# Optimization experiments

Measured on AMD Instinct MI355X. Metric: run time of the kernel, lower is better.

Reference implementation:

```python
import jax, jax.numpy as jnp
import numpy as np

D_MODEL = 1024
NHEAD = 16
HEAD_DIM = D_MODEL // NHEAD
WINDOW = 64


def setup_inputs() -> dict:
    key = jax.random.key(0)
    ks = jax.random.split(key, 5)
    B, S = 1, 4096
    x = jax.random.normal(ks[0], (B, S, D_MODEL), dtype=jnp.float32)
    scale = 0.02
    Wq = jax.random.normal(ks[1], (D_MODEL, D_MODEL), dtype=jnp.float32) * scale
    Wk = jax.random.normal(ks[2], (D_MODEL, D_MODEL), dtype=jnp.float32) * scale
    Wv = jax.random.normal(ks[3], (D_MODEL, D_MODEL), dtype=jnp.float32) * scale
    Wo = jax.random.normal(ks[4], (D_MODEL, D_MODEL), dtype=jnp.float32) * scale
    return {"x": x, "Wq": Wq, "Wk": Wk, "Wv": Wv, "Wo": Wo}


def reference(x, Wq, Wk, Wv, Wo):
    B, S, D = x.shape
    H, hd, W = NHEAD, HEAD_DIM, WINDOW
    # projections (torch Linear: y = x @ W.T)
    q = (x @ Wq.T).reshape(B, S, H, hd).transpose(0, 2, 1, 3)  # [B,H,S,hd]
    k = (x @ Wk.T).reshape(B, S, H, hd).transpose(0, 2, 1, 3)
    v = (x @ Wv.T).reshape(B, S, H, hd).transpose(0, 2, 1, 3)
    # sliding window indices: each query attends to [i-W+1, i]
    qpos = jnp.arange(S)
    offsets = jnp.arange(-W + 1, 1)
    key_idx = qpos[:, None] + offsets[None, :]          # [S,W]
    valid = (key_idx >= 0) & (key_idx < S)
    key_idx = jnp.clip(key_idx, 0, S - 1)
    # gather windows: [B,H,S,W,hd]
    kw = jnp.take(k, key_idx, axis=2)
    vw = jnp.take(v, key_idx, axis=2)
    scores = jnp.einsum('bhsd,bhswd->bhsw', q, kw) / (hd ** 0.5)
    scores = jnp.where(valid[None, None, :, :], scores, -jnp.inf)
    attn = jax.nn.softmax(scores, axis=-1)
    out = jnp.einsum('bhsw,bhswd->bhsd', attn, vw)      # [B,H,S,hd]
    out = out.transpose(0, 2, 1, 3).reshape(B, S, D)
    return out @ Wo.T
```

## Files before the change

kernel.cpp:

```cpp
#include <hip/hip_runtime.h>
#include <cstdint>

typedef unsigned short u16;
using bf16x8 = __attribute__((ext_vector_type(8))) short;
using u16x8  = __attribute__((ext_vector_type(8))) unsigned short;
using f32x4  = __attribute__((ext_vector_type(4))) float;

#define DM 1024

__device__ __forceinline__ u16 f2b(float f) {
    union { float f; unsigned u; } v; v.f = f;
    unsigned r = v.u + 0x7FFFu + ((v.u >> 16) & 1u);
    return (u16)(r >> 16);
}
__device__ __forceinline__ float b2f(u16 b) {
    union { unsigned u; float f; } v; v.u = ((unsigned)b) << 16;
    return v.f;
}

#define GLL(gp, lp) __builtin_amdgcn_global_load_lds( \
    (const __attribute__((address_space(1))) void*)(uintptr_t)(gp), \
    (__attribute__((address_space(3))) void*)(unsigned)(uintptr_t)(lp), 16, 0, 0)

#define BAR()    __builtin_amdgcn_s_barrier()
#define WAITV3() asm volatile("s_waitcnt vmcnt(3)" ::: "memory")
#define WAITV0() asm volatile("s_waitcnt vmcnt(0)" ::: "memory")

__global__ __launch_bounds__(256) void cvt_all(const float* __restrict__ x,
                                               const float* __restrict__ Wq,
                                               const float* __restrict__ Wk,
                                               const float* __restrict__ Wv,
                                               const float* __restrict__ Wo,
                                               u16* __restrict__ xb,
                                               u16* __restrict__ wqkv,
                                               u16* __restrict__ wob) {
    size_t v = ((size_t)blockIdx.x * 256 + threadIdx.x) << 3;
    const float* src; u16* dst; size_t off;
    if (v < (size_t)4194304) { src = x; dst = xb; off = v; }
    else {
        size_t w = v - 4194304; int s = (int)(w >> 20); off = w & 1048575;
        src = (s == 0) ? Wq : (s == 1) ? Wk : (s == 2) ? Wv : Wo;
        dst = (s < 3) ? (wqkv + ((size_t)s << 20)) : wob;
    }
    const f32x4* p = (const f32x4*)(src + off);
    f32x4 a = p[0], b = p[1];
    u16x8 o;
    o[0] = f2b(a[0]); o[1] = f2b(a[1]); o[2] = f2b(a[2]); o[3] = f2b(a[3]);
    o[4] = f2b(b[0]); o[5] = f2b(b[1]); o[6] = f2b(b[2]); o[7] = f2b(b[3]);
    *(u16x8*)(dst + off) = o;
}

#define MROW3(af_, bf_, d) \
    acc[d][0] = __builtin_amdgcn_mfma_f32_16x16x32_bf16(af_, bf_[0], acc[d][0], 0, 0, 0); \
    acc[d][1] = __builtin_amdgcn_mfma_f32_16x16x32_bf16(af_, bf_[1], acc[d][1], 0, 0, 0); \
    acc[d][2] = __builtin_amdgcn_mfma_f32_16x16x32_bf16(af_, bf_[2], acc[d][2], 0, 0, 0);

#define MFMA12(af_, bf_, ib) do { \
    __builtin_amdgcn_s_setprio(1); \
    MROW3(af_[0], bf_, (ib) + 0) \
    MROW3(af_[1], bf_, (ib) + 1) \
    MROW3(af_[2], bf_, (ib) + 2) \
    MROW3(af_[3], bf_, (ib) + 3) \
    __builtin_amdgcn_s_setprio(0); } while (0)

__global__ __launch_bounds__(512, 2) void gemm_qkv8(const u16* __restrict__ A,
                                                    const u16* __restrict__ B,
                                                    u16* __restrict__ QKV) {
    __shared__ __align__(16) u16 As[2 * 16384];
    __shared__ __align__(16) u16 Bs[2 * 12288];
    const int tid  = threadIdx.x;
    const int lane = tid & 63;
    const int wid  = tid >> 6;
    const int wr   = wid >> 2;
    const int wc   = wid & 3;
    const int fr   = lane & 15;
    const int fg   = lane >> 4;

    const int hw   = blockIdx.y * 16 + blockIdx.x;
    const int lg   = (hw & 7) * 32 + (hw >> 3);
    const int brow = (lg >> 4) << 8;
    const int bcol = (lg & 15) * 192;

    const int srow = tid >> 3;
    const int scol = ((tid & 7) ^ (srow & 7)) << 3;
    const u16* Ag = A + (size_t)(brow + srow) * 1024 + scol;
    const u16* Bg = B + (size_t)(bcol + srow) * 1024 + scol;

#define STG_A(buf, kt, c) GLL(Ag + (size_t)(c) * 65536 + (kt) * 64, \
                              (char*)As + (buf) * 32768 + (c) * 8192 + (wid << 10))
#define STG_B(buf, kt, c) GLL(Bg + (size_t)(c) * 65536 + (kt) * 64, \
                              (char*)Bs + (buf) * 24576 + (c) * 8192 + (wid << 10))

    const int swz  = (fr & 7) << 3;
    const int col0 = (fg << 3) ^ swz;
    const int col1 = (32 + (fg << 3)) ^ swz;
    const int aro  = ((wr << 7) + fr) << 6;
    const int bro  = ((wc * 48) + fr) << 6;

#define LDA4(dst, bufo, ih, cl) do { \
    const u16* p_ = As + (bufo) + aro + ((ih) << 12) + (cl); \
    dst[0] = *(const bf16x8*)(p_); \
    dst[1] = *(const bf16x8*)(p_ + 1024); \
    dst[2] = *(const bf16x8*)(p_ + 2048); \
    dst[3] = *(const bf16x8*)(p_ + 3072); } while (0)

#define LDB3(dst, bufo, cl) do { \
    const u16* p_ = Bs + (bufo) + bro + (cl); \
    dst[0] = *(const bf16x8*)(p_); \
    dst[1] = *(const bf16x8*)(p_ + 1024); \
    dst[2] = *(const bf16x8*)(p_ + 2048); } while (0)

    f32x4 acc[8][3];
    const f32x4 z = {0.f, 0.f, 0.f, 0.f};
    #pragma unroll
    for (int i = 0; i < 8; ++i)
        #pragma unroll
        for (int j = 0; j < 3; ++j) acc[i][j] = z;

    bf16x8 af0[4], af1[4], bf0[3], bf1[3];

    STG_B(0, 0, 0); STG_B(0, 0, 1); STG_B(0, 0, 2);
    STG_A(0, 0, 0); STG_A(0, 0, 1); STG_A(0, 0, 2); STG_A(0, 0, 3);
    STG_B(1, 1, 0); STG_B(1, 1, 1); STG_B(1, 1, 2);
    WAITV3();
    BAR();

    #pragma unroll 1
    for (int t = 0; t < 7; ++t) {
        const int k1 = 2 * t + 1, k2 = 2 * t + 2, k3 = 2 * t + 3;
        LDA4(af0, 0, 0, col0); LDB3(bf0, 0, col0);
        STG_A(1, k1, 0); STG_A(1, k1, 1);
        BAR(); MFMA12(af0, bf0, 0); BAR();
        LDA4(af1, 0, 0, col1); LDB3(bf1, 0, col1);
        STG_A(1, k1, 2); STG_A(1, k1, 3);
        BAR(); MFMA12(af1, bf1, 0); BAR();
        LDA4(af0, 0, 1, col0);
        STG_B(0, k2, 0); STG_B(0, k2, 1);
        BAR(); MFMA12(af0, bf0, 4); BAR();
        LDA4(af1, 0, 1, col1);
        STG_B(0, k2, 2);
        BAR(); MFMA12(af1, bf1, 4); WAITV3(); BAR();
        LDA4(af0, 16384, 0, col0); LDB3(bf0, 12288, col0);
        STG_A(0, k2, 0); STG_A(0, k2, 1);
        BAR(); MFMA12(af0, bf0, 0); BAR();
        LDA4(af1, 16384, 0, col1); LDB3(bf1, 12288, col1);
        STG_A(0, k2, 2); STG_A(0, k2, 3);
        BAR(); MFMA12(af1, bf1, 0); BAR();
        LDA4(af0, 16384, 1, col0);
        STG_B(1, k3, 0); STG_B(1, k3, 1);
        BAR(); MFMA12(af0, bf0, 4); BAR();
        LDA4(af1, 16384, 1, col1);
        STG_B(1, k3, 2);
        BAR(); MFMA12(af1, bf1, 4); WAITV3(); BAR();
    }
    LDA4(af0, 0, 0, col0); LDB3(bf0, 0, col0);
    STG_A(1, 15, 0); STG_A(1, 15, 1);
    BAR(); MFMA12(af0, bf0, 0); BAR();
    LDA4(af1, 0, 0, col1); LDB3(bf1, 0, col1);
    STG_A(1, 15, 2); STG_A(1, 15, 3);
    BAR(); MFMA12(af1, bf1, 0); BAR();
    LDA4(af0, 0, 1, col0);
    BAR(); MFMA12(af0, bf0, 4); BAR();
    LDA4(af1, 0, 1, col1);
    BAR(); MFMA12(af1, bf1, 4); WAITV0(); BAR();
    LDA4(af0, 16384, 0, col0); LDB3(bf0, 12288, col0);
    BAR(); MFMA12(af0, bf0, 0); BAR();
    LDA4(af1, 16384, 0, col1); LDB3(bf1, 12288, col1);
    BAR(); MFMA12(af1, bf1, 0); BAR();
    LDA4(af0, 16384, 1, col0);
    BAR(); MFMA12(af0, bf0, 4); BAR();
    LDA4(af1, 16384, 1, col1);
    BAR(); MFMA12(af1, bf1, 4);

    const int ocol0 = bcol + wc * 48;
    const int orow0 = brow + (wr << 7);
    #pragma unroll
    for (int i = 0; i < 8; ++i)
        #pragma unroll
        for (int j = 0; j < 3; ++j)
            #pragma unroll
            for (int r = 0; r < 4; ++r) {
                const int row = orow0 + i * 16 + fg * 4 + r;
                const int col = ocol0 + j * 16 + fr;
                QKV[(size_t)row * 3072 + col] = f2b(acc[i][j][r]);
            }
#undef STG_A
#undef STG_B
#undef LDA4
#undef LDB3
}

__global__ __launch_bounds__(256) void gemm_out(const u16* __restrict__ A,
                                                const u16* __restrict__ B,
                                                float* __restrict__ C) {
    __shared__ __align__(16) u16 As[2 * 8192];
    __shared__ __align__(16) u16 Bs[2 * 4096];
    const int tid  = threadIdx.x;
    const int lane = tid & 63;
    const int wid  = tid >> 6;
    const int wr   = wid >> 1;
    const int wc   = wid & 1;
    const int fr   = lane & 15;
    const int fg   = lane >> 4;

    const int hw   = blockIdx.y * 16 + blockIdx.x;
    const int lg   = (hw & 7) * 64 + (hw >> 3);
    const int brow = (lg >> 4) << 7;
    const int bcol = (lg & 15) << 6;

    const int srow = tid >> 3;
    const int scol = ((tid & 7) ^ (srow & 7)) << 3;
    const u16* Ag = A + (size_t)(brow + srow) * 1024 + scol;
    const u16* Bg = B + (size_t)(bcol + srow) * 1024 + scol;

#define OSTG_A(buf, kt, c) GLL(Ag + (size_t)(c) * 32768 + (kt) * 64, \
                               (char*)As + (buf) * 16384 + (c) * 4096 + (tid << 4))
#define OSTG_B(buf, kt, c) GLL(Bg + (size_t)(c) * 32768 + (kt) * 64, \
                               (char*)Bs + (buf) * 8192 + (c) * 4096 + (tid << 4))
#define OSTG(buf, kt) do { \
        OSTG_A(buf, kt, 0); OSTG_A(buf, kt, 1); OSTG_A(buf, kt, 2); OSTG_A(buf, kt, 3); \
        OSTG_B(buf, kt, 0); OSTG_B(buf, kt, 1); } while (0)

    const int swz  = (fr & 7) << 3;
    const int col0 = (fg << 3) ^ swz;
    const int col1 = (32 + (fg << 3)) ^ swz;
    const int aro  = ((wr << 6) + fr) << 6;
    const int bro  = ((wc << 5) + fr) << 6;

    f32x4 acc[4][2];
    const f32x4 z = {0.f, 0.f, 0.f, 0.f};
    #pragma unroll
    for (int i = 0; i < 4; ++i) { acc[i][0] = z; acc[i][1] = z; }

    OSTG(0, 0);
    #pragma unroll 2
    for (int kt = 0; kt < 16; ++kt) {
        const int buf = kt & 1;
        __syncthreads();
        if (kt + 1 < 16) OSTG(buf ^ 1, kt + 1);
        const u16* Ab = As + (buf << 13);
        const u16* Bb = Bs + (buf << 12);
        bf16x8 a0[4], a1[4], b0[2], b1[2];
        #pragma unroll
        for (int i = 0; i < 4; ++i) {
            a0[i] = *(const bf16x8*)(Ab + aro + (i << 10) + col0);
            a1[i] = *(const bf16x8*)(Ab + aro + (i << 10) + col1);
        }
        #pragma unroll
        for (int j = 0; j < 2; ++j) {
            b0[j] = *(const bf16x8*)(Bb + bro + (j << 10) + col0);
            b1[j] = *(const bf16x8*)(Bb + bro + (j << 10) + col1);
        }
        #pragma unroll
        for (int i = 0; i < 4; ++i)
            #pragma unroll
            for (int j = 0; j < 2; ++j) {
                acc[i][j] = __builtin_amdgcn_mfma_f32_16x16x32_bf16(a0[i], b0[j], acc[i][j], 0, 0, 0);
                acc[i][j] = __builtin_amdgcn_mfma_f32_16x16x32_bf16(a1[i], b1[j], acc[i][j], 0, 0, 0);
            }
    }
#undef OSTG_A
#undef OSTG_B
#undef OSTG

    #pragma unroll
    for (int i = 0; i < 4; ++i)
        #pragma unroll
        for (int j = 0; j < 2; ++j)
            #pragma unroll
            for (int r = 0; r < 4; ++r) {
                const int row = brow + wr * 64 + i * 16 + fg * 4 + r;
                const int col = bcol + wc * 32 + j * 16 + fr;
                C[(size_t)row * 1024 + col] = acc[i][j][r];
            }
}

__global__ __launch_bounds__(256) void attn_kernel(const u16* __restrict__ QKV,
                                                   u16* __restrict__ Og) {
    const int qb  = blockIdx.x;
    const int h   = blockIdx.y;
    const int tid = threadIdx.x;
    const int lane = tid & 63;
    const int w  = tid >> 6;
    const int fr = lane & 15;
    const int fg = lane >> 4;

    __shared__ __align__(16) u16 QK[64 * 72 + 128 * 72];
    __shared__ __align__(16) u16 Vt[64 * 138];
    __shared__ float Mrow[64][4];
    __shared__ float Lrow[64][4];

    u16* Qs = QK;
    u16* Ks = QK + 64 * 72;
    u16* Ps = QK;

    const u16* Qg = QKV;
    const u16* Kg = QKV + 1024;
    const u16* Vg = QKV + 2048;

    const int hoff  = h * 64;
    const int qrow0 = qb * 64;
    const int krow0 = qrow0 - 64;

    {
        const int r  = tid >> 3;
        const int c0 = (tid & 7) * 8;
        #pragma unroll
        for (int it = 0; it < 2; ++it) {
            const int row = r + it * 32;
            u16x8 val = *(const u16x8*)(Qg + (size_t)(qrow0 + row) * 3072 + hoff + c0);
            u16x8 o;
            #pragma unroll
            for (int e = 0; e < 8; ++e) o[e] = f2b(b2f(val[e]) * 0.125f);
            *(u16x8*)(Qs + row * 72 + c0) = o;
        }
        #pragma unroll
        for (int it = 0; it < 4; ++it) {
            const int row  = r + it * 32;
            const int grow = krow0 + row;
            u16x8 val = {0, 0, 0, 0, 0, 0, 0, 0};
            if (grow >= 0) val = *(const u16x8*)(Kg + (size_t)grow * 3072 + hoff + c0);
            *(u16x8*)(Ks + row * 72 + c0) = val;
        }
        #pragma unroll
        for (int it = 0; it < 4; ++it) {
            const int j    = r + it * 32;
            const int grow = krow0 + j;
            u16x8 val = {0, 0, 0, 0, 0, 0, 0, 0};
            if (grow >= 0) val = *(const u16x8*)(Vg + (size_t)grow * 3072 + hoff + c0);
            #pragma unroll
            for (int e = 0; e < 8; ++e) Vt[(c0 + e) * 138 + j] = val[e];
        }
    }
    __syncthreads();

    const f32x4 z = {0.f, 0.f, 0.f, 0.f};
    f32x4 s[4][2];
    #pragma unroll
    for (int i = 0; i < 4; ++i) { s[i][0] = z; s[i][1] = z; }
    #pragma unroll
    for (int kk = 0; kk < 2; ++kk) {
        const int k0 = kk * 32 + fg * 8;
        bf16x8 aq[4];
        #pragma unroll
        for (int i = 0; i < 4; ++i)
            aq[i] = *(const bf16x8*)(Qs + (i * 16 + fr) * 72 + k0);
        #pragma unroll
        for (int n = 0; n < 2; ++n) {
            const bf16x8 bk = *(const bf16x8*)(Ks + (w * 32 + n * 16 + fr) * 72 + k0);
            #pragma unroll
            for (int i = 0; i < 4; ++i)
                s[i][n] = __builtin_amdgcn_mfma_f32_16x16x32_bf16(aq[i], bk, s[i][n], 0, 0, 0);
        }
    }

    #pragma unroll
    for (int i = 0; i < 4; ++i) {
        #pragma unroll
        for (int r = 0; r < 4; ++r) {
            const int irow = i * 16 + fg * 4 + r;
            float mx = -3.0e38f;
            #pragma unroll
            for (int n = 0; n < 2; ++n) {
                const int jcol = w * 32 + n * 16 + fr;
                const bool valid = (jcol >= irow + 1) && (jcol <= irow + 64) && (krow0 + jcol >= 0);
                const float v = valid ? s[i][n][r] : -3.0e38f;
                s[i][n][r] = v;
                mx = fmaxf(mx, v);
            }
            #pragma unroll
            for (int d = 1; d < 16; d <<= 1) mx = fmaxf(mx, __shfl_xor(mx, d));
            if (fr == 0) Mrow[irow][w] = mx;
        }
    }
    __syncthreads();

    #pragma unroll
    for (int i = 0; i < 4; ++i) {
        #pragma unroll
        for (int r = 0; r < 4; ++r) {
            const int irow = i * 16 + fg * 4 + r;
            const float M = fmaxf(fmaxf(Mrow[irow][0], Mrow[irow][1]),
                                  fmaxf(Mrow[irow][2], Mrow[irow][3]));
            float sum = 0.f;
            #pragma unroll
            for (int n = 0; n < 2; ++n) {
                const float v = s[i][n][r];
                const float p = (v > -1.0e38f) ? __expf(v - M) : 0.f;
                sum += p;
                Ps[irow * 136 + (w * 32 + n * 16 + fr)] = f2b(p);
            }
            #pragma unroll
            for (int d = 1; d < 16; d <<= 1) sum += __shfl_xor(sum, d);
            if (fr == 0) Lrow[irow][w] = sum;
        }
    }
    __syncthreads();

    f32x4 o[4] = {z, z, z, z};
    #pragma unroll
    for (int ks = 0; ks < 4; ++ks) {
        const int k0 = ks * 32 + fg * 8;
        const bf16x8 ap = *(const bf16x8*)(Ps + (w * 16 + fr) * 136 + k0);
        #pragma unroll
        for (int n = 0; n < 4; ++n) {
            const bf16x8 bv = *(const bf16x8*)(Vt + (n * 16 + fr) * 138 + k0);
            o[n] = __builtin_amdgcn_mfma_f32_16x16x32_bf16(ap, bv, o[n], 0, 0, 0);
        }
    }

    #pragma unroll
    for (int r = 0; r < 4; ++r) {
        const int irow = w * 16 + fg * 4 + r;
        const float L = Lrow[irow][0] + Lrow[irow][1] + Lrow[irow][2] + Lrow[irow][3];
        const float rl = 1.0f / L;
        #pragma unroll
        for (int n = 0; n < 4; ++n)
            Og[(size_t)(qrow0 + irow) * DM + hoff + n * 16 + fr] = f2b(o[n][r] * rl);
    }
}

extern "C" void kernel_launch(void* const* d_in, const int* in_sizes, int n_in,
                              void* d_out, int out_size, void* d_ws, size_t ws_size,
                              hipStream_t stream) {
    (void)in_sizes; (void)n_in; (void)out_size; (void)ws_size;
    const float* x  = (const float*)d_in[0];
    const float* Wq = (const float*)d_in[1];
    const float* Wk = (const float*)d_in[2];
    const float* Wv = (const float*)d_in[3];
    const float* Wo = (const float*)d_in[4];
    float* out = (float*)d_out;

    char* ws = (char*)d_ws;
    u16* xb   = (u16*)(ws);
    u16* Wqkv = (u16*)(ws + ((size_t)8  << 20));
    u16* Wob  = (u16*)(ws + ((size_t)14 << 20));
    u16* qkvb = (u16*)(ws + ((size_t)16 << 20));
    u16* ab   = (u16*)(ws + ((size_t)40 << 20));

    cvt_all<<<4096, 256, 0, stream>>>(x, Wq, Wk, Wv, Wo, xb, Wqkv, Wob);
    gemm_qkv8<<<dim3(16, 16), 512, 0, stream>>>(xb, Wqkv, qkvb);
    attn_kernel<<<dim3(64, 16), 256, 0, stream>>>(qkvb, ab);
    gemm_out<<<dim3(16, 32), 256, 0, stream>>>(ab, Wob, out);
}
```

Baseline: 80.79 us.

## Restructure QKV GEMM main loop into simpler double-buffered pipeline, fold Q scale into Wq

```diff
diff --git a/kernel.cpp b/kernel.cpp
--- a/kernel.cpp
+++ b/kernel.cpp
@@ -23,7 +23,7 @@
     (__attribute__((address_space(3))) void*)(unsigned)(uintptr_t)(lp), 16, 0, 0)
 
 #define BAR()    __builtin_amdgcn_s_barrier()
-#define WAITV3() asm volatile("s_waitcnt vmcnt(3)" ::: "memory")
+#define WAITV7() asm volatile("s_waitcnt vmcnt(7)" ::: "memory")
 #define WAITV0() asm volatile("s_waitcnt vmcnt(0)" ::: "memory")
 
 __global__ __launch_bounds__(256) void cvt_all(const float* __restrict__ x,
@@ -35,18 +35,19 @@
                                                u16* __restrict__ wqkv,
                                                u16* __restrict__ wob) {
     size_t v = ((size_t)blockIdx.x * 256 + threadIdx.x) << 3;
-    const float* src; u16* dst; size_t off;
+    const float* src; u16* dst; size_t off; float sc = 1.0f;
     if (v < (size_t)4194304) { src = x; dst = xb; off = v; }
     else {
         size_t w = v - 4194304; int s = (int)(w >> 20); off = w & 1048575;
         src = (s == 0) ? Wq : (s == 1) ? Wk : (s == 2) ? Wv : Wo;
         dst = (s < 3) ? (wqkv + ((size_t)s << 20)) : wob;
+        if (s == 0) sc = 0.125f;
     }
     const f32x4* p = (const f32x4*)(src + off);
     f32x4 a = p[0], b = p[1];
     u16x8 o;
-    o[0] = f2b(a[0]); o[1] = f2b(a[1]); o[2] = f2b(a[2]); o[3] = f2b(a[3]);
-    o[4] = f2b(b[0]); o[5] = f2b(b[1]); o[6] = f2b(b[2]); o[7] = f2b(b[3]);
+    o[0] = f2b(a[0] * sc); o[1] = f2b(a[1] * sc); o[2] = f2b(a[2] * sc); o[3] = f2b(a[3] * sc);
+    o[4] = f2b(b[0] * sc); o[5] = f2b(b[1] * sc); o[6] = f2b(b[2] * sc); o[7] = f2b(b[3] * sc);
     *(u16x8*)(dst + off) = o;
 }
 
@@ -55,12 +56,16 @@
     acc[d][1] = __builtin_amdgcn_mfma_f32_16x16x32_bf16(af_, bf_[1], acc[d][1], 0, 0, 0); \
     acc[d][2] = __builtin_amdgcn_mfma_f32_16x16x32_bf16(af_, bf_[2], acc[d][2], 0, 0, 0);
 
-#define MFMA12(af_, bf_, ib) do { \
+#define MFMA24(ib) do { \
     __builtin_amdgcn_s_setprio(1); \
-    MROW3(af_[0], bf_, (ib) + 0) \
-    MROW3(af_[1], bf_, (ib) + 1) \
-    MROW3(af_[2], bf_, (ib) + 2) \
-    MROW3(af_[3], bf_, (ib) + 3) \
+    MROW3(af0[0], bf0, (ib) + 0) \
+    MROW3(af0[1], bf0, (ib) + 1) \
+    MROW3(af0[2], bf0, (ib) + 2) \
+    MROW3(af0[3], bf0, (ib) + 3) \
+    MROW3(af1[0], bf1, (ib) + 0) \
+    MROW3(af1[1], bf1, (ib) + 1) \
+    MROW3(af1[2], bf1, (ib) + 2) \
+    MROW3(af1[3], bf1, (ib) + 3) \
     __builtin_amdgcn_s_setprio(0); } while (0)
 
 __global__ __launch_bounds__(512, 2) void gemm_qkv8(const u16* __restrict__ A,
@@ -119,58 +124,39 @@
 
     bf16x8 af0[4], af1[4], bf0[3], bf1[3];
 
+    STG_A(0, 0, 0); STG_A(0, 0, 1); STG_A(0, 0, 2); STG_A(0, 0, 3);
     STG_B(0, 0, 0); STG_B(0, 0, 1); STG_B(0, 0, 2);
-    STG_A(0, 0, 0); STG_A(0, 0, 1); STG_A(0, 0, 2); STG_A(0, 0, 3);
+    STG_A(1, 1, 0); STG_A(1, 1, 1); STG_A(1, 1, 2); STG_A(1, 1, 3);
     STG_B(1, 1, 0); STG_B(1, 1, 1); STG_B(1, 1, 2);
-    WAITV3();
-    BAR();
 
     #pragma unroll 1
-    for (int t = 0; t < 7; ++t) {
-        const int k1 = 2 * t + 1, k2 = 2 * t + 2, k3 = 2 * t + 3;
-        LDA4(af0, 0, 0, col0); LDB3(bf0, 0, col0);
-        STG_A(1, k1, 0); STG_A(1, k1, 1);
-        BAR(); MFMA12(af0, bf0, 0); BAR();
-        LDA4(af1, 0, 0, col1); LDB3(bf1, 0, col1);
-        STG_A(1, k1, 2); STG_A(1, k1, 3);
-        BAR(); MFMA12(af1, bf1, 0); BAR();
-        LDA4(af0, 0, 1, col0);
-        STG_B(0, k2, 0); STG_B(0, k2, 1);
-        BAR(); MFMA12(af0, bf0, 4); BAR();
-        LDA4(af1, 0, 1, col1);
-        STG_B(0, k2, 2);
-        BAR(); MFMA12(af1, bf1, 4); WAITV3(); BAR();
-        LDA4(af0, 16384, 0, col0); LDB3(bf0, 12288, col0);
-        STG_A(0, k2, 0); STG_A(0, k2, 1);
-        BAR(); MFMA12(af0, bf0, 0); BAR();
-        LDA4(af1, 16384, 0, col1); LDB3(bf1, 12288, col1);
-        STG_A(0, k2, 2); STG_A(0, k2, 3);
-        BAR(); MFMA12(af1, bf1, 0); BAR();
-        LDA4(af0, 16384, 1, col0);
-        STG_B(1, k3, 0); STG_B(1, k3, 1);
-        BAR(); MFMA12(af0, bf0, 4); BAR();
-        LDA4(af1, 16384, 1, col1);
-        STG_B(1, k3, 2);
-        BAR(); MFMA12(af1, bf1, 4); WAITV3(); BAR();
-    }
-    LDA4(af0, 0, 0, col0); LDB3(bf0, 0, col0);
-    STG_A(1, 15, 0); STG_A(1, 15, 1);
-    BAR(); MFMA12(af0, bf0, 0); BAR();
-    LDA4(af1, 0, 0, col1); LDB3(bf1, 0, col1);
-    STG_A(1, 15, 2); STG_A(1, 15, 3);
-    BAR(); MFMA12(af1, bf1, 0); BAR();
-    LDA4(af0, 0, 1, col0);
-    BAR(); MFMA12(af0, bf0, 4); BAR();
-    LDA4(af1, 0, 1, col1);
-    BAR(); MFMA12(af1, bf1, 4); WAITV0(); BAR();
-    LDA4(af0, 16384, 0, col0); LDB3(bf0, 12288, col0);
-    BAR(); MFMA12(af0, bf0, 0); BAR();
-    LDA4(af1, 16384, 0, col1); LDB3(bf1, 12288, col1);
-    BAR(); MFMA12(af1, bf1, 0); BAR();
-    LDA4(af0, 16384, 1, col0);
-    BAR(); MFMA12(af0, bf0, 4); BAR();
-    LDA4(af1, 16384, 1, col1);
-    BAR(); MFMA12(af1, bf1, 4);
+    for (int t = 0; t < 14; ++t) {
+        const int bo  = (t & 1) ? 16384 : 0;
+        const int bob = (t & 1) ? 12288 : 0;
+        WAITV7();
+        BAR();
+        LDA4(af0, bo, 0, col0); LDA4(af1, bo, 0, col1);
+        LDB3(bf0, bob, col0);   LDB3(bf1, bob, col1);
+        MFMA24(0);
+        LDA4(af0, bo, 1, col0); LDA4(af1, bo, 1, col1);
+        MFMA24(4);
+        BAR();
+        STG_A(t & 1, t + 2, 0); STG_A(t & 1, t + 2, 1);
+        STG_A(t & 1, t + 2, 2); STG_A(t & 1, t + 2, 3);
+        STG_B(t & 1, t + 2, 0); STG_B(t & 1, t + 2, 1); STG_B(t & 1, t + 2, 2);
+    }
+    WAITV7(); BAR();
+    LDA4(af0, 0, 0, col0); LDA4(af1, 0, 0, col1);
+    LDB3(bf0, 0, col0);    LDB3(bf1, 0, col1);
+    MFMA24(0);
+    LDA4(af0, 0, 1, col0); LDA4(af1, 0, 1, col1);
+    MFMA24(4);
+    WAITV0(); BAR();
+    LDA4(af0, 16384, 0, col0); LDA4(af1, 16384, 0, col1);
+    LDB3(bf0, 12288, col0);    LDB3(bf1, 12288, col1);
+    MFMA24(0);
+    LDA4(af0, 16384, 1, col0); LDA4(af1, 16384, 1, col1);
+    MFMA24(4);
 
     const int ocol0 = bcol + wc * 48;
     const int orow0 = brow + (wr << 7);
@@ -309,10 +295,7 @@
         for (int it = 0; it < 2; ++it) {
             const int row = r + it * 32;
             u16x8 val = *(const u16x8*)(Qg + (size_t)(qrow0 + row) * 3072 + hoff + c0);
-            u16x8 o;
-            #pragma unroll
-            for (int e = 0; e < 8; ++e) o[e] = f2b(b2f(val[e]) * 0.125f);
-            *(u16x8*)(Qs + row * 72 + c0) = o;
+            *(u16x8*)(Qs + row * 72 + c0) = val;
         }
         #pragma unroll
         for (int it = 0; it < 4; ++it) {
```

Measured after the change: 80.96 us. No clear change (+0.2%).
